# Kernel tuning notes

Hardware: AMD Instinct MI355X
Metric: run time of the kernel (lower is better)

## Reference

```python
import jax, jax.numpy as jnp
import numpy as np

ANG, CEN = 9, 4
MIND, MAXD = -4, 4
NDISP = MAXD - MIND + 1
BDR = CEN * MAXD  # 16
EPS = 1e-5


def lrelu(x):
    return jnp.where(x >= 0, x, 0.1 * x)


def bn(x, p):
    # p: [4, C] = (gamma, beta, running_mean, running_var); inference-mode BatchNorm
    g, b, m, v = p
    sh = (1, -1) + (1,) * (x.ndim - 2)
    return (x - m.reshape(sh)) * (g.reshape(sh) * jax.lax.rsqrt(v.reshape(sh) + EPS)) + b.reshape(sh)


def conv3d(x, w, pad):
    return jax.lax.conv_general_dilated(
        x, w, (1, 1, 1), [(pad[0], pad[0]), (pad[1], pad[1]), (pad[2], pad[2])],
        dimension_numbers=('NCDHW', 'OIDHW', 'NCDHW'))


def pw3d(x, w, b=None):  # 1x1x1 conv
    y = jnp.einsum('oc,bcdhw->bodhw', w, x)
    return y if b is None else y + b.reshape(1, -1, 1, 1, 1)


def bilinear_zeros(img, px, py):
    # torch F.grid_sample(mode='bilinear', padding_mode='zeros', align_corners=False)
    # img [..., h, w]; px, py: same leading dims + [h, w] (pixel coords)
    h, w = img.shape[-2], img.shape[-1]
    x0 = jnp.floor(px); y0 = jnp.floor(py)
    dx = px - x0; dy = py - y0
    x0i = x0.astype(jnp.int32); y0i = y0.astype(jnp.int32)
    flat = img.reshape(img.shape[:-2] + (h * w,))

    def tap(yi, xi, wgt):
        valid = ((xi >= 0) & (xi < w) & (yi >= 0) & (yi < h)).astype(img.dtype)
        idx = jnp.clip(yi, 0, h - 1) * w + jnp.clip(xi, 0, w - 1)
        v = jnp.take_along_axis(flat, idx.reshape(idx.shape[:-2] + (h * w,)), axis=-1)
        return v.reshape(idx.shape) * wgt * valid

    return (tap(y0i, x0i, (1 - dx) * (1 - dy)) + tap(y0i, x0i + 1, dx * (1 - dy)) +
            tap(y0i + 1, x0i, (1 - dx) * dy) + tap(y0i + 1, x0i + 1, dx * dy))


def generate_mask(lf, disp):
    # lf [b,1,9,9,h,w]; warp() is called with -disp in the torch code
    b, _, _, _, h, w = lf.shape
    imgs = lf[:, 0]                                    # [b,9,9,h,w]
    d = -disp[:, 0]                                    # [b,h,w]
    off = (jnp.arange(ANG) - CEN).astype(imgs.dtype)   # du / dv
    xb = jnp.linspace(0.0, 1.0, w).astype(imgs.dtype)
    yb = jnp.linspace(0.0, 1.0, h).astype(imgs.dtype)
    # grid = 2*(base+shift)-1; align_corners=False pixel coord = ((g+1)*S - 1)/2
    px = (xb[None, None, None, :] + off[None, :, None, None] * d[:, None] / w) * w - 0.5  # [b,9(v),h,w]
    py = (yb[None, None, :, None] + off[None, :, None, None] * d[:, None] / h) * h - 0.5  # [b,9(u),h,w]
    PX = jnp.broadcast_to(px[:, None], (b, ANG, ANG, h, w))
    PY = jnp.broadcast_to(py[:, :, None], (b, ANG, ANG, h, w))
    warped = bilinear_zeros(imgs, PX, PY)
    ref = imgs[:, CEN, CEN][:, None, None]
    diff = jnp.abs(warped - ref)
    diff = diff.at[:, CEN, CEN].set(0.0)  # center view is used unwarped -> zero diff
    return ((1.0 - diff) ** 2).reshape(b, ANG * ANG, h, w)


def build_cost(feat, mask, fuse_w):
    # Direct windowed gather equivalent of the per-disparity Unfold(dilation=h_pad-d)
    # on the angular-tiled padded image. For disparity d and view (ki,kj), output
    # pixel (i,j) reads view (ki,kj) at (i+(CEN-ki)*d, j+(CEN-kj)*d), zeros outside.
    b, c, _, h, w = feat.shape                        # feat [b,8,81,h,w]
    f = feat.reshape(b, c, ANG, ANG, h, w)
    fpad = jnp.pad(f, ((0, 0), (0, 0), (0, 0), (0, 0), (BDR, BDR), (BDR, BDR)))
    ds = jnp.arange(MIND, MAXD + 1)                   # [9]
    ki = jnp.arange(ANG)
    row = BDR + (CEN - ki)[None, :, None] * ds[:, None, None] + jnp.arange(h)[None, None, :]  # [D,9,h]
    col = BDR + (CEN - ki)[None, :, None] * ds[:, None, None] + jnp.arange(w)[None, None, :]  # [D,9,w]
    KI = ki[None, :, None, None, None]
    KJ = ki[None, None, :, None, None]
    RR = row[:, :, None, :, None]
    CC = col[:, None, :, None, :]
    g = fpad[:, :, KI, KJ, RR, CC]                    # [b,8,D,9,9,h,w]
    mod = g * mask.reshape(b, 1, 1, ANG, ANG, h, w)   # mask modulation (ModulateConv2d)
    Wf = fuse_w.reshape(c, fuse_w.shape[0] // c, ANG, ANG)  # grouped 1x1 fuse, groups=c
    cost = jnp.einsum('gouv,bgduvhw->bgodhw', Wf, mod).reshape(b, fuse_w.shape[0], NDISP, h, w)
    return cost / mask.mean(axis=1)[:, None, None]


def _forward(x, dispGT, if_w0, if_bn0, resb_w, resb_b, resb_bn, if_w1, if_bn1,
             if_w2, if_bn2, last_w, fuse_w, sq_w, sq_bn, c1_w, c1_bn, c2_w, c2_bn,
             c3_w, c3_bn, c4_w, r3_body_w, r3_body_bn, r3_ca_w1, r3_ca_b1, r3_ca_bn1,
             r3_ca_w2, r3_ca_b2, r3_ca_bn2):
    b = x.shape[0]
    h = x.shape[2] // ANG; w = x.shape[3] // ANG
    lf = x.reshape(b, 1, ANG, h, ANG, w).transpose(0, 1, 2, 4, 3, 5)  # [b,1,a1,a2,h,w]
    x5 = lf.reshape(b, 1, ANG * ANG, h, w)
    # ---- init_feature: per-view 2D convs expressed as (1,3,3) 3D convs
    hbuf = bn(conv3d(x5, if_w0, (0, 1, 1)), if_bn0)
    for i in range(8):  # 8 ResB blocks (fixed architecture depth)
        t = lrelu(bn(conv3d(hbuf, resb_w[i, 0], (0, 1, 1)) + resb_b[i, 0].reshape(1, -1, 1, 1, 1), resb_bn[i, 0]))
        t = bn(conv3d(t, resb_w[i, 1], (0, 1, 1)) + resb_b[i, 1].reshape(1, -1, 1, 1, 1), resb_bn[i, 1])
        hbuf = hbuf + t
    hbuf = lrelu(bn(conv3d(hbuf, if_w1, (0, 1, 1)), if_bn1))
    hbuf = lrelu(bn(conv3d(hbuf, if_w2, (0, 1, 1)), if_bn2))
    feat = conv3d(hbuf, last_w, (0, 1, 1))            # [b,8,81,h,w]
    # ---- occlusion-aware mask + cost volume
    mask = generate_mask(lf, dispGT)                  # [b,81,h,w]
    cost = build_cost(feat, mask, fuse_w)             # [b,512,9,h,w]
    # ---- 3D CNN aggregation
    buf = lrelu(bn(pw3d(cost, sq_w), sq_bn))
    buf = lrelu(bn(conv3d(buf, c1_w, (1, 1, 1)), c1_bn))
    buf = lrelu(bn(conv3d(buf, c2_w, (1, 1, 1)), c2_bn))
    for i in range(2):  # ResB3D blocks with CALayer
        t = lrelu(bn(conv3d(buf, r3_body_w[i, 0], (1, 1, 1)), r3_body_bn[i, 0]))
        t = bn(conv3d(t, r3_body_w[i, 1], (1, 1, 1)), r3_body_bn[i, 1])
        y = t.mean(axis=(3, 4), keepdims=True)        # AdaptiveAvgPool3d((9,1,1))
        y = lrelu(bn(pw3d(y, r3_ca_w1[i], r3_ca_b1[i]), r3_ca_bn1[i]))
        y = jax.nn.sigmoid(bn(pw3d(y, r3_ca_w2[i], r3_ca_b2[i]), r3_ca_bn2[i]))
        buf = t * y + buf
    buf = lrelu(bn(conv3d(buf, c3_w, (1, 1, 1)), c3_bn))
    score = conv3d(buf, c4_w, (1, 1, 1))[:, 0]        # [b,9,h,w]
    att = jax.nn.softmax(score, axis=1)
    dvals = jnp.arange(MIND, MAXD + 1).astype(att.dtype)
    return jnp.sum(att * dvals[None, :, None, None], axis=1, keepdims=True)  # [b,1,h,w]


def setup_inputs():
    B, H, W = 1, 64, 64
    keys = iter(jax.random.split(jax.random.key(0), 256))

    def nrm(shape, fan_in):
        return jax.random.normal(next(keys), shape, jnp.float32) / np.float32(np.sqrt(fan_in))

    def bnp(c):
        k1, k2, k3, k4 = jax.random.split(next(keys), 4)
        return jnp.stack([jax.random.uniform(k1, (c,), jnp.float32, 0.5, 1.5),
                          0.1 * jax.random.normal(k2, (c,), jnp.float32),
                          0.1 * jax.random.normal(k3, (c,), jnp.float32),
                          jax.random.uniform(k4, (c,), jnp.float32, 0.5, 1.5)])

    d = {}
    d['x'] = jax.random.normal(next(keys), (B, 1, ANG * H, ANG * W), jnp.float32)
    d['dispGT'] = jax.random.uniform(next(keys), (B, 1, H, W), jnp.float32, -4.0, 4.0)
    d['if_w0'] = nrm((16, 1, 1, 3, 3), 9)
    d['if_bn0'] = bnp(16)
    d['resb_w'] = nrm((8, 2, 16, 16, 1, 3, 3), 16 * 9)
    d['resb_b'] = 0.01 * jax.random.normal(next(keys), (8, 2, 16), jnp.float32)
    d['resb_bn'] = jnp.stack([jnp.stack([bnp(16), bnp(16)]) for _ in range(8)])
    d['if_w1'] = nrm((16, 16, 1, 3, 3), 16 * 9)
    d['if_bn1'] = bnp(16)
    d['if_w2'] = nrm((8, 16, 1, 3, 3), 16 * 9)
    d['if_bn2'] = bnp(8)
    d['last_w'] = nrm((8, 8, 1, 3, 3), 8 * 9)
    d['fuse_w'] = nrm((512, 81), 81)
    d['sq_w'] = nrm((160, 512), 512)
    d['sq_bn'] = bnp(160)
    for nmn in ('c1', 'c2', 'c3'):
        d[nmn + '_w'] = nrm((160, 160, 3, 3, 3), 160 * 27)
        d[nmn + '_bn'] = bnp(160)
    d['c4_w'] = nrm((1, 160, 3, 3, 3), 160 * 27)
    d['r3_body_w'] = nrm((2, 2, 160, 160, 3, 3, 3), 160 * 27)
    d['r3_body_bn'] = jnp.stack([jnp.stack([bnp(160), bnp(160)]) for _ in range(2)])
    d['r3_ca_w1'] = nrm((2, 10, 160), 160)
    d['r3_ca_b1'] = 0.01 * jax.random.normal(next(keys), (2, 10), jnp.float32)
    d['r3_ca_bn1'] = jnp.stack([bnp(10) for _ in range(2)])
    d['r3_ca_w2'] = nrm((2, 160, 10), 10)
    d['r3_ca_b2'] = 0.01 * jax.random.normal(next(keys), (2, 160), jnp.float32)
    d['r3_ca_bn2'] = jnp.stack([bnp(160) for _ in range(2)])
    return d


def reference(x, dispGT, if_w0, if_bn0, resb_w, resb_b, resb_bn, if_w1, if_bn1,
              if_w2, if_bn2, last_w, fuse_w, sq_w, sq_bn, c1_w, c1_bn, c2_w, c2_bn,
              c3_w, c3_bn, c4_w, r3_body_w, r3_body_bn, r3_ca_w1, r3_ca_b1, r3_ca_bn1,
              r3_ca_w2, r3_ca_b2, r3_ca_bn2):
    return _forward(x, dispGT, if_w0, if_bn0, resb_w, resb_b, resb_bn, if_w1, if_bn1,
                    if_w2, if_bn2, last_w, fuse_w, sq_w, sq_bn, c1_w, c1_bn, c2_w, c2_bn,
                    c3_w, c3_bn, c4_w, r3_body_w, r3_body_bn, r3_ca_w1, r3_ca_b1, r3_ca_bn1,
                    r3_ca_w2, r3_ca_b2, r3_ca_bn2)
```

## Files before the change

### kernel.cpp

```cpp
#include <hip/hip_runtime.h>
#include <hip/hip_bf16.h>
#include <math.h>

constexpr float EPSB = 1e-5f;

constexpr int SAS = 69696;
constexpr int SRS = 1056;
constexpr size_t SVOL = 81ull * SAS;

constexpr int PZS = 696960;
constexpr int PYS = 10560;
constexpr size_t PVOL = 11ull * 4356 * 160;

constexpr size_t OFF_SA   = 0;
constexpr size_t OFF_SB   = 5645376;
constexpr size_t OFF_MASK = 11290752;
constexpr size_t OFF_INVM = 11622528;
constexpr size_t OFF_SC   = 11626624;
constexpr size_t OFF_YM   = 11663488;
constexpr size_t OFF_Y2   = 11664928;
constexpr size_t OFF_YMP  = 11666368;
constexpr size_t OFF_PA   = 11712448;
constexpr size_t UOFF_PHA = 38758016;
constexpr size_t UOFF_PHB = 46424576;
constexpr size_t UOFF_WH  = 54091136;
constexpr size_t UOFF_WSH = 63767936;
constexpr size_t UOFF_ABH = 63865216;
constexpr size_t UOFF_ABL = 63972736;

typedef short s16x8 __attribute__((ext_vector_type(8)));
typedef short s16x4 __attribute__((ext_vector_type(4)));
typedef float f32x4 __attribute__((ext_vector_type(4)));
typedef _Float16 h16x8 __attribute__((ext_vector_type(8)));
typedef _Float16 h16x4 __attribute__((ext_vector_type(4)));

__device__ __forceinline__ float lrelu_f(float v) { return v >= 0.f ? v : 0.1f * v; }
__device__ __forceinline__ float b2f(unsigned short s) {
  union { float f; unsigned u; } z; z.u = ((unsigned)s) << 16; return z.f;
}
__device__ __forceinline__ unsigned short f2b(float f) {
  __hip_bfloat16 h = __float2bfloat16(f);
  return *(unsigned short*)&h;
}

__global__ __launch_bounds__(256) void k_if0(const float* __restrict__ x,
                                             const float* __restrict__ w0,
                                             const float* __restrict__ bn0,
                                             float* __restrict__ SA) {
  int a = blockIdx.x;
  int p = blockIdx.y * 256 + threadIdx.x;
  int y = p >> 6, xx = p & 63;
  int ai = a / 9, aj = a % 9;
  float v[3][3];
#pragma unroll
  for (int dy = 0; dy < 3; ++dy) {
    int gy = y + dy - 1;
#pragma unroll
    for (int dx = 0; dx < 3; ++dx) {
      int gx = xx + dx - 1;
      v[dy][dx] = (gy >= 0 && gy < 64 && gx >= 0 && gx < 64)
                      ? x[(ai * 64 + gy) * 576 + aj * 64 + gx] : 0.f;
    }
  }
  float o16[16];
#pragma unroll
  for (int c = 0; c < 16; ++c) {
    float acc = 0.f;
#pragma unroll
    for (int t = 0; t < 9; ++t) acc += w0[c * 9 + t] * v[t / 3][t % 3];
    float g = bn0[c], b = bn0[16 + c], m = bn0[32 + c], vv = bn0[48 + c];
    o16[c] = (acc - m) * (g * rsqrtf(vv + EPSB)) + b;
  }
  float* dst = SA + (size_t)a * SAS + (size_t)(y + 1) * SRS + (size_t)(xx + 1) * 16;
#pragma unroll
  for (int q = 0; q < 4; ++q)
    *(float4*)&dst[q * 4] = make_float4(o16[q*4], o16[q*4+1], o16[q*4+2], o16[q*4+3]);
}

__global__ __launch_bounds__(256) void k_wslice(const float* __restrict__ resb_w,
                                                const float* __restrict__ if1_w,
                                                const float* __restrict__ if2_w,
                                                const float* __restrict__ last_w,
                                                _Float16* __restrict__ WSH) {
  int c = blockIdx.x;
  for (int idx = threadIdx.x; idx < 2560; idx += 256) {
    int o = idx / 160, k = idx % 160;
    int t = k >> 4, ci = k & 15;
    float v = 0.f;
    if (t < 9) {
      if (c < 16)       v = resb_w[((size_t)c * 256 + o * 16 + ci) * 9 + t];
      else if (c == 16) v = if1_w[(size_t)(o * 16 + ci) * 9 + t];
      else if (c == 17) v = (o < 8) ? if2_w[(size_t)(o * 16 + ci) * 9 + t] : 0.f;
      else              v = (o < 8 && ci < 8) ? last_w[(size_t)(o * 8 + ci) * 9 + t] : 0.f;
    }
    WSH[c * 2560 + idx] = (_Float16)v;
  }
}

__global__ __launch_bounds__(256) void k_wt7(const float* __restrict__ c1,
                                             const float* __restrict__ c2,
                                             const float* __restrict__ r3,
                                             const float* __restrict__ c3,
                                             _Float16* __restrict__ WH) {
  __shared__ float L[6912];
  int l = blockIdx.y;
  const float* w = (l == 0) ? c1 : (l == 1) ? c2 : (l < 6) ? r3 + (size_t)(l - 2) * 691200 : c3;
  size_t base = (size_t)blockIdx.x * 256;
  for (int i = threadIdx.x; i < 6912; i += 256) L[i] = w[base * 27 + i];
  __syncthreads();
  _Float16* wh = WH + (size_t)l * 691200;
  int r = (int)base + threadIdx.x;
#pragma unroll 1
  for (int t = 0; t < 27; ++t) {
    float v = L[threadIdx.x * 27 + t];
    wh[(size_t)t * 25600 + r] = (_Float16)v;
  }
}

__global__ __launch_bounds__(192) void k_A(const float* __restrict__ sq_w,
                                           const float* __restrict__ fuse_w,
                                           unsigned short* __restrict__ ABH,
                                           unsigned short* __restrict__ ABL) {
  int k = blockIdx.x;
  int o = threadIdx.x;
  if (o >= 160) return;
  float acc = 0.f;
  if (k < 648) {
    int uv = k >> 3, g = k & 7;
    for (int o2 = 0; o2 < 64; ++o2)
      acc += sq_w[(size_t)o * 512 + g * 64 + o2] * fuse_w[(size_t)(g * 64 + o2) * 81 + uv];
  }
  unsigned short h = f2b(acc);
  ABH[(size_t)o * 672 + k] = h;
  ABL[(size_t)o * 672 + k] = f2b(acc - b2f(h));
}

__device__ __forceinline__ float img_at(const float* __restrict__ x, int i, int j, int yy, int xx) {
  if (yy < 0 || yy >= 64 || xx < 0 || xx >= 64) return 0.f;
  return x[(i * 64 + yy) * 576 + j * 64 + xx];
}

__global__ __launch_bounds__(256) void k_mask(const float* __restrict__ x,
                                              const float* __restrict__ disp,
                                              float* __restrict__ mask,
                                              float* __restrict__ invm) {
  int p = blockIdx.x * 256 + threadIdx.x;
  int y = p >> 6, xx = p & 63;
  float d = -disp[p];
  float ref = x[(4 * 64 + y) * 576 + 4 * 64 + xx];
  float ssum = 0.f;
  float xbase = (float)xx * (64.0f / 63.0f);
  float ybase = (float)y * (64.0f / 63.0f);
  for (int i = 0; i < 9; ++i) {
    float py = ybase + (float)(i - 4) * d - 0.5f;
    float y0f = floorf(py);
    float fy = py - y0f;
    int y0 = (int)y0f;
    for (int j = 0; j < 9; ++j) {
      float px = xbase + (float)(j - 4) * d - 0.5f;
      float x0f = floorf(px);
      float fx = px - x0f;
      int x0 = (int)x0f;
      float val = img_at(x, i, j, y0, x0) * (1.f - fx) * (1.f - fy)
                + img_at(x, i, j, y0, x0 + 1) * fx * (1.f - fy)
                + img_at(x, i, j, y0 + 1, x0) * (1.f - fx) * fy
                + img_at(x, i, j, y0 + 1, x0 + 1) * fx * fy;
      float diff = (i == 4 && j == 4) ? 0.f : fabsf(val - ref);
      float m = 1.f - diff;
      m = m * m;
      mask[(i * 9 + j) * 4096 + p] = m;
      ssum += m;
    }
  }
  invm[p] = 81.f / ssum;
}

template <bool BN, bool LRELU, bool RESADD, int CO>
__global__ __launch_bounds__(256) void k_cs(const float* __restrict__ in,
                                            float* __restrict__ out,
                                            const _Float16* __restrict__ wsh,
                                            const float* __restrict__ bias,
                                            const float* __restrict__ bnp) {
  __shared__ _Float16 Af[15840];
  int a = blockIdx.x, y0 = blockIdx.y * 8;
  int tid = threadIdx.x, lane = tid & 63, w = tid >> 6;
  int lr = lane & 15, lq = lane >> 4;
  const float* src = in + (size_t)a * SAS + (size_t)y0 * SRS;
  for (int it = tid; it < 2640; it += 256) {
    int row = it / 264, rem = it % 264;
    float4 f = *(const float4*)&src[row * SRS + rem * 4];
    int px = rem >> 2, q = rem & 3;
    h16x4 hv;
    hv[0] = (_Float16)f.x;
    hv[1] = (_Float16)f.y;
    hv[2] = (_Float16)f.z;
    hv[3] = (_Float16)f.w;
    *(h16x4*)&Af[(row * 66 + px) * 24 + q * 4] = hv;
  }
  __syncthreads();
  h16x8 bh[5];
#pragma unroll
  for (int ks = 0; ks < 5; ++ks)
    bh[ks] = *(const h16x8*)&wsh[lr * 160 + ks * 32 + lq * 8];
  int offk[5];
#pragma unroll
  for (int ks = 0; ks < 5; ++ks) {
    int t = ks * 2 + (lq >> 1);
    if (t > 8) t = 8;
    offk[ks] = ((t / 3) * 66 + (t % 3)) * 24 + (lq & 1) * 8;
  }
  f32x4 acc[8];
#pragma unroll
  for (int i = 0; i < 8; ++i) acc[i] = (f32x4){0.f, 0.f, 0.f, 0.f};
#pragma unroll
  for (int mf = 0; mf < 8; ++mf) {
    int gm = w * 8 + mf;
    int yl = gm >> 2, xq = gm & 3;
    int am = (yl * 66 + xq * 16 + lr) * 24;
#pragma unroll
    for (int ks = 0; ks < 5; ++ks) {
      h16x8 ah = *(const h16x8*)&Af[am + offk[ks]];
      acc[mf] = __builtin_amdgcn_mfma_f32_16x16x32_f16(ah, bh[ks], acc[mf], 0, 0, 0);
    }
  }
  int co = lr;
  bool coval = (CO == 16) || (co < CO);
  float sc = 1.f, sh = 0.f;
  if (BN && coval) {
    float g = bnp[co], b = bnp[CO + co], m = bnp[2 * CO + co], vv = bnp[3 * CO + co];
    sc = g * rsqrtf(vv + EPSB);
    sh = b - m * sc;
    if (bias) sh += bias[co] * sc;
  }
#pragma unroll
  for (int mf = 0; mf < 8; ++mf) {
    int gm = w * 8 + mf;
    int yl = gm >> 2, xq = gm & 3;
    if (coval) {
#pragma unroll
      for (int r = 0; r < 4; ++r) {
        int x = xq * 16 + lq * 4 + r;
        float val = acc[mf][r] * sc + sh;
        if (LRELU) val = lrelu_f(val);
        size_t oo = (size_t)a * SAS + (size_t)(y0 + yl + 1) * SRS + (size_t)(x + 1) * 16 + co;
        if (RESADD) out[oo] += val;
        else        out[oo] = val;
      }
    }
  }
}

__global__ __launch_bounds__(256) void k_costsq(const float* __restrict__ feat,
                                                const float* __restrict__ mask,
                                                const float* __restrict__ invm,
                                                const unsigned short* __restrict__ ABH,
                                                const unsigned short* __restrict__ ABL,
                                                const float* __restrict__ sq_bn,
                                                _Float16* __restrict__ outPH) {
  __shared__ short Ah[6144];
  __shared__ short Al[6144];
  int dI = blockIdx.x, y = blockIdx.y;
  int dd = dI - 4;
  int tid = threadIdx.x, lane = tid & 63, w = tid >> 6;
  int wm = w >> 1, wn = w & 1;
  int lr = lane & 15, lq = lane >> 4;
  f32x4 acc[2][5];
#pragma unroll
  for (int i = 0; i < 2; ++i)
#pragma unroll
    for (int j = 0; j < 5; ++j) acc[i][j] = (f32x4){0.f, 0.f, 0.f, 0.f};

  for (int ch = 0; ch < 7; ++ch) {
    __syncthreads();
    for (int it = tid; it < 768; it += 256) {
      int xl = it / 12, uvL = it % 12;
      int uv = ch * 12 + uvL;
      s16x8 hv = {0, 0, 0, 0, 0, 0, 0, 0}, lv = {0, 0, 0, 0, 0, 0, 0, 0};
      if (uv < 81) {
        int u = uv / 9, v = uv % 9;
        int ys = y + (4 - u) * dd;
        int xs = xl + (4 - v) * dd;
        if (ys >= 0 && ys < 64 && xs >= 0 && xs < 64) {
          const float* fp = feat + (size_t)uv * SAS + (size_t)(ys + 1) * SRS + (size_t)(xs + 1) * 16;
          float mv = mask[uv * 4096 + y * 64 + xl];
#pragma unroll
          for (int j = 0; j < 8; ++j) {
            float f = fp[j] * mv;
            unsigned short h = f2b(f);
            hv[j] = h;
            lv[j] = f2b(f - b2f(h));
          }
        }
      }
      *(s16x8*)&Ah[xl * 96 + uvL * 8] = hv;
      *(s16x8*)&Al[xl * 96 + uvL * 8] = lv;
    }
    __syncthreads();
#pragma unroll
    for (int kb = 0; kb < 3; ++kb) {
      int ka = kb * 32 + lq * 8;
      s16x8 a0h = *(const s16x8*)&Ah[(wm * 32 + lr) * 96 + ka];
      s16x8 a0l = *(const s16x8*)&Al[(wm * 32 + lr) * 96 + ka];
      s16x8 a1h = *(const s16x8*)&Ah[(wm * 32 + 16 + lr) * 96 + ka];
      s16x8 a1l = *(const s16x8*)&Al[(wm * 32 + 16 + lr) * 96 + ka];
      int kg = ch * 96 + ka;
#pragma unroll
      for (int nf = 0; nf < 5; ++nf) {
        int n = wn * 80 + nf * 16 + lr;
        s16x8 bh = *(const s16x8*)&ABH[(size_t)n * 672 + kg];
        s16x8 bl = *(const s16x8*)&ABL[(size_t)n * 672 + kg];
        acc[0][nf] = __builtin_amdgcn_mfma_f32_16x16x32_bf16(a0h, bh, acc[0][nf], 0, 0, 0);
        acc[0][nf] = __builtin_amdgcn_mfma_f32_16x16x32_bf16(a0h, bl, acc[0][nf], 0, 0, 0);
        acc[0][nf] = __builtin_amdgcn_mfma_f32_16x16x32_bf16(a0l, bh, acc[0][nf], 0, 0, 0);
        acc[1][nf] = __builtin_amdgcn_mfma_f32_16x16x32_bf16(a1h, bh, acc[1][nf], 0, 0, 0);
        acc[1][nf] = __builtin_amdgcn_mfma_f32_16x16x32_bf16(a1h, bl, acc[1][nf], 0, 0, 0);
        acc[1][nf] = __builtin_amdgcn_mfma_f32_16x16x32_bf16(a1l, bh, acc[1][nf], 0, 0, 0);
      }
    }
  }
#pragma unroll
  for (int nf = 0; nf < 5; ++nf) {
    int n = wn * 80 + nf * 16 + lr;
    float g = sq_bn[n], b = sq_bn[160 + n], m = sq_bn[320 + n], vv = sq_bn[480 + n];
    float sc = g * rsqrtf(vv + EPSB), sh = b - m * sc;
#pragma unroll
    for (int mf = 0; mf < 2; ++mf) {
#pragma unroll
      for (int r = 0; r < 4; ++r) {
        int x = wm * 32 + mf * 16 + lq * 4 + r;
        float val = acc[mf][nf][r] * invm[y * 64 + x];
        val = val * sc + sh;
        val = lrelu_f(val);
        outPH[(size_t)(dI + 1) * PZS + (size_t)(y + 1) * PYS + (size_t)(x + 1) * 160 + n] =
            (_Float16)val;
      }
    }
  }
}

template <bool LRELU>
__global__ __launch_bounds__(320, 3) void k_mconv(const _Float16* __restrict__ in,
                                                  float* __restrict__ out32,
                                                  _Float16* __restrict__ out16,
                                                  const _Float16* __restrict__ wh,
                                                  const float* __restrict__ bnp) {
  __shared__ _Float16 Af[66 * 168];
  int bid = blockIdx.x;
  int swz = (bid & 7) * 72 + (bid >> 3);
  int z = swz / 64, y = swz % 64;
  int tid = threadIdx.x;
  int lane = tid & 63;
  int wn = tid >> 6;
  int lr = lane & 15;
  int lq = lane >> 4;

  f32x4 acc[4][2];
#pragma unroll
  for (int i = 0; i < 4; ++i)
#pragma unroll
    for (int j = 0; j < 2; ++j) acc[i][j] = (f32x4){0.f, 0.f, 0.f, 0.f};

  const _Float16* wbase = wh + (size_t)(wn * 32 + lr) * 160 + lq * 8;

#pragma unroll 1
  for (int dzy = 0; dzy < 9; ++dzy) {
    int dz = dzy / 3, dy = dzy % 3;
    const _Float16* src = in + (size_t)(z + dz) * PZS + (size_t)(y + dy) * PYS;
    __syncthreads();
    for (int v = tid; v < 1320; v += 320) {
      h16x8 g = *(const h16x8*)&src[(size_t)v * 8];
      int row = v / 20, col = (v % 20) * 8;
      *(h16x8*)&Af[row * 168 + col] = g;
    }
    __syncthreads();

#pragma unroll 1
    for (int dx = 0; dx < 3; ++dx) {
      const _Float16* wt = wbase + (size_t)(dzy * 3 + dx) * 25600;
      h16x8 bA[2], bB[2];
#pragma unroll
      for (int nf = 0; nf < 2; ++nf)
        bA[nf] = *(const h16x8*)&wt[(size_t)nf * 16 * 160];

      auto step = [&](int ks, h16x8 (&cur)[2], h16x8 (&nxt)[2], bool pre) {
        if (pre) {
#pragma unroll
          for (int nf = 0; nf < 2; ++nf)
            nxt[nf] = *(const h16x8*)&wt[(size_t)nf * 16 * 160 + (ks + 1) * 32];
        }
        h16x8 a0 = *(const h16x8*)&Af[(0 * 16 + lr + dx) * 168 + ks * 32 + lq * 8];
        h16x8 a1 = *(const h16x8*)&Af[(1 * 16 + lr + dx) * 168 + ks * 32 + lq * 8];
        h16x8 a2 = *(const h16x8*)&Af[(2 * 16 + lr + dx) * 168 + ks * 32 + lq * 8];
        h16x8 a3 = *(const h16x8*)&Af[(3 * 16 + lr + dx) * 168 + ks * 32 + lq * 8];
#pragma unroll
        for (int nf = 0; nf < 2; ++nf) {
          acc[0][nf] = __builtin_amdgcn_mfma_f32_16x16x32_f16(a0, cur[nf], acc[0][nf], 0, 0, 0);
          acc[1][nf] = __builtin_amdgcn_mfma_f32_16x16x32_f16(a1, cur[nf], acc[1][nf], 0, 0, 0);
          acc[2][nf] = __builtin_amdgcn_mfma_f32_16x16x32_f16(a2, cur[nf], acc[2][nf], 0, 0, 0);
          acc[3][nf] = __builtin_amdgcn_mfma_f32_16x16x32_f16(a3, cur[nf], acc[3][nf], 0, 0, 0);
        }
      };
      step(0, bA, bB, true);
      step(1, bB, bA, true);
      step(2, bA, bB, true);
      step(3, bB, bA, true);
      step(4, bA, bB, false);
    }
  }
#pragma unroll
  for (int nf = 0; nf < 2; ++nf) {
    int n = wn * 32 + nf * 16 + lr;
    float sc = bnp[n] * rsqrtf(bnp[480 + n] + EPSB);
    float sh = bnp[160 + n] - bnp[320 + n] * sc;
#pragma unroll
    for (int mq = 0; mq < 4; ++mq) {
#pragma unroll
      for (int r = 0; r < 4; ++r) {
        int x = mq * 16 + lq * 4 + r;
        float val = acc[mq][nf][r] * sc + sh;
        if (LRELU) val = lrelu_f(val);
        size_t oo = (size_t)(z + 1) * PZS + (size_t)(y + 1) * PYS + (size_t)(x + 1) * 160 + n;
        if (out32) out32[oo] = val;
        if (out16) out16[oo] = (_Float16)val;
      }
    }
  }
}

__global__ __launch_bounds__(256) void k_c4(const _Float16* __restrict__ in,
                                            const float* __restrict__ w,
                                            float* __restrict__ score) {
  __shared__ float L[66 * 169];
  __shared__ float red[256];
  int zy = blockIdx.x;
  int z = zy / 64, y = zy % 64;
  int tid = threadIdx.x;
  int x = tid & 63, q = tid >> 6;
  float acc = 0.f;
  for (int dzy = 0; dzy < 9; ++dzy) {
    int dz = dzy / 3, dy = dzy % 3;
    const _Float16* src = in + (size_t)(z + dz) * PZS + (size_t)(y + dy) * PYS;
    __syncthreads();
    for (int v = tid; v < 1320; v += 256) {
      h16x8 g = *(const h16x8*)&src[v * 8];
      int row = v / 20, col = (v % 20) * 8;
#pragma unroll
      for (int j = 0; j < 8; ++j) L[row * 169 + col + j] = (float)g[j];
    }
    __syncthreads();
#pragma unroll 1
    for (int dx = 0; dx < 3; ++dx) {
      int t = dzy * 3 + dx;
      for (int ci = q * 40; ci < q * 40 + 40; ++ci)
        acc += L[(x + dx) * 169 + ci] * w[ci * 27 + t];
    }
  }
  red[tid] = acc;
  __syncthreads();
  if (q == 0)
    score[z * 4096 + y * 64 + x] = red[x] + red[64 + x] + red[128 + x] + red[192 + x];
}

__global__ __launch_bounds__(256) void k_mean1(const float* __restrict__ in,
                                               float* __restrict__ ymp) {
  int z = blockIdx.x, yg = blockIdx.y, xq = blockIdx.z;
  int c = threadIdx.x;
  if (c >= 160) return;
  float s = 0.f;
  for (int yy = 0; yy < 8; ++yy) {
    int y = yg * 8 + yy;
    for (int xl = 0; xl < 16; ++xl) {
      int x = xq * 16 + xl;
      s += in[(size_t)(z + 1) * PZS + (size_t)(y + 1) * PYS + (size_t)(x + 1) * 160 + c];
    }
  }
  ymp[((z * 8 + yg) * 4 + xq) * 160 + c] = s;
}

__global__ __launch_bounds__(256) void k_mean2(const float* __restrict__ ymp,
                                               float* __restrict__ ym) {
  int idx = blockIdx.x * 256 + threadIdx.x;
  if (idx >= 1440) return;
  int c = idx / 9, z = idx % 9;
  float s = 0.f;
  for (int p = 0; p < 32; ++p) s += ymp[(z * 32 + p) * 160 + c];
  ym[idx] = s * (1.f / 4096.f);
}

__global__ __launch_bounds__(256) void k_ca(const float* __restrict__ ym,
                                            const float* __restrict__ w1,
                                            const float* __restrict__ b1,
                                            const float* __restrict__ bn1,
                                            const float* __restrict__ w2,
                                            const float* __restrict__ b2,
                                            const float* __restrict__ bn2,
                                            float* __restrict__ y2) {
  __shared__ float yml[1440];
  __shared__ float yy[90];
  for (int i = threadIdx.x; i < 1440; i += 256) yml[i] = ym[i];
  __syncthreads();
  if (threadIdx.x < 90) {
    int c = threadIdx.x / 9, z = threadIdx.x % 9;
    float acc = b1[c];
    for (int ci = 0; ci < 160; ++ci) acc += w1[c * 160 + ci] * yml[ci * 9 + z];
    float g = bn1[c], b = bn1[10 + c], m = bn1[20 + c], vv = bn1[30 + c];
    acc = (acc - m) * (g * rsqrtf(vv + EPSB)) + b;
    yy[threadIdx.x] = lrelu_f(acc);
  }
  __syncthreads();
  for (int i = threadIdx.x; i < 1440; i += 256) {
    int c = i / 9, z = i % 9;
    float acc = b2[c];
#pragma unroll
    for (int k = 0; k < 10; ++k) acc += w2[c * 10 + k] * yy[k * 9 + z];
    float g = bn2[c], b = bn2[160 + c], m = bn2[320 + c], vv = bn2[480 + c];
    acc = (acc - m) * (g * rsqrtf(vv + EPSB)) + b;
    y2[i] = 1.f / (1.f + expf(-acc));
  }
}

__global__ __launch_bounds__(256) void k_sadd(float* __restrict__ buf,
                                              _Float16* __restrict__ shadow,
                                              const float* __restrict__ t,
                                              const float* __restrict__ y2) {
  int i = blockIdx.x * 256 + threadIdx.x;
  int p = i / 160, c = i % 160;
  int z = p >> 12, r = p & 4095;
  int y = r >> 6, x = r & 63;
  size_t a = (size_t)(z + 1) * PZS + (size_t)(y + 1) * PYS + (size_t)(x + 1) * 160 + c;
  float val = buf[a] + t[a] * y2[c * 9 + z];
  buf[a] = val;
  shadow[a] = (_Float16)val;
}

__global__ __launch_bounds__(256) void k_out(const float* __restrict__ score,
                                             float* __restrict__ out) {
  int p = blockIdx.x * 256 + threadIdx.x;
  float v[9];
  float mx = -1e30f;
#pragma unroll
  for (int z = 0; z < 9; ++z) {
    v[z] = score[z * 4096 + p];
    mx = fmaxf(mx, v[z]);
  }
  float s = 0.f, r = 0.f;
#pragma unroll
  for (int z = 0; z < 9; ++z) {
    float e = expf(v[z] - mx);
    s += e;
    r += e * (float)(z - 4);
  }
  out[p] = r / s;
}

extern "C" void kernel_launch(void* const* d_in, const int* in_sizes, int n_in,
                              void* d_out, int out_size, void* d_ws, size_t ws_size,
                              hipStream_t stream) {
  const float* X      = (const float*)d_in[0];
  const float* disp   = (const float*)d_in[1];
  const float* if_w0  = (const float*)d_in[2];
  const float* if_bn0 = (const float*)d_in[3];
  const float* resb_w = (const float*)d_in[4];
  const float* resb_b = (const float*)d_in[5];
  const float* resb_bn= (const float*)d_in[6];
  const float* if_w1  = (const float*)d_in[7];
  const float* if_bn1 = (const float*)d_in[8];
  const float* if_w2  = (const float*)d_in[9];
  const float* if_bn2 = (const float*)d_in[10];
  const float* last_w = (const float*)d_in[11];
  const float* fuse_w = (const float*)d_in[12];
  const float* sq_w   = (const float*)d_in[13];
  const float* sq_bn  = (const float*)d_in[14];
  const float* c1_w   = (const float*)d_in[15];
  const float* c1_bn  = (const float*)d_in[16];
  const float* c2_w   = (const float*)d_in[17];
  const float* c2_bn  = (const float*)d_in[18];
  const float* c3_w   = (const float*)d_in[19];
  const float* c3_bn  = (const float*)d_in[20];
  const float* c4_w   = (const float*)d_in[21];
  const float* r3_w   = (const float*)d_in[22];
  const float* r3_bn  = (const float*)d_in[23];
  const float* ca_w1  = (const float*)d_in[24];
  const float* ca_b1  = (const float*)d_in[25];
  const float* ca_bn1 = (const float*)d_in[26];
  const float* ca_w2  = (const float*)d_in[27];
  const float* ca_b2  = (const float*)d_in[28];
  const float* ca_bn2 = (const float*)d_in[29];

  float* ws   = (float*)d_ws;
  float* SA   = ws + OFF_SA;
  float* SB   = ws + OFF_SB;
  float* PC   = ws;
  float* MASK = ws + OFF_MASK;
  float* INVM = ws + OFF_INVM;
  float* SC   = ws + OFF_SC;
  float* YM   = ws + OFF_YM;
  float* Y2   = ws + OFF_Y2;
  float* YMP  = ws + OFF_YMP;
  float* PA   = ws + OFF_PA;
  unsigned short* U   = (unsigned short*)d_ws;
  _Float16* PHA       = (_Float16*)(U + UOFF_PHA);
  _Float16* PHB       = (_Float16*)(U + UOFF_PHB);
  _Float16* WH        = (_Float16*)(U + UOFF_WH);
  _Float16* WSS       = (_Float16*)(U + UOFF_WSH);
  unsigned short* ABH = U + UOFF_ABH;
  unsigned short* ABL = U + UOFF_ABL;

  hipMemsetAsync(SA, 0, SVOL * 4, stream);
  hipMemsetAsync(SB, 0, SVOL * 4, stream);
  hipMemsetAsync(PHA, 0, PVOL * 2, stream);
  hipMemsetAsync(PHB, 0, PVOL * 2, stream);

  k_wt7<<<dim3(100, 7), 256, 0, stream>>>(c1_w, c2_w, r3_w, c3_w, WH);
  k_wslice<<<19, 256, 0, stream>>>(resb_w, if_w1, if_w2, last_w, WSS);
  k_A<<<672, 192, 0, stream>>>(sq_w, fuse_w, ABH, ABL);
  k_mask<<<16, 256, 0, stream>>>(X, disp, MASK, INVM);

  k_if0<<<dim3(81, 16), 256, 0, stream>>>(X, if_w0, if_bn0, SA);
  for (int i = 0; i < 8; ++i) {
    k_cs<true, true, false, 16><<<dim3(81, 8), 256, 0, stream>>>(
        SA, SB, WSS + (size_t)(2 * i) * 2560, resb_b + i * 32, resb_bn + i * 128);
    k_cs<true, false, true, 16><<<dim3(81, 8), 256, 0, stream>>>(
        SB, SA, WSS + (size_t)(2 * i + 1) * 2560, resb_b + i * 32 + 16, resb_bn + i * 128 + 64);
  }
  k_cs<true, true, false, 16><<<dim3(81, 8), 256, 0, stream>>>(
      SA, SB, WSS + 16 * 2560, nullptr, if_bn1);
  k_cs<true, true, false, 8><<<dim3(81, 8), 256, 0, stream>>>(
      SB, SA, WSS + 17 * 2560, nullptr, if_bn2);
  k_cs<false, false, false, 8><<<dim3(81, 8), 256, 0, stream>>>(
      SA, SB, WSS + 18 * 2560, nullptr, nullptr);

  k_costsq<<<dim3(9, 64), 256, 0, stream>>>(SB, MASK, INVM, ABH, ABL, sq_bn, PHA);

  k_mconv<true><<<576, 320, 0, stream>>>(PHA, nullptr, PHB, WH + 0ull * 691200, c1_bn);
  k_mconv<true><<<576, 320, 0, stream>>>(PHB, PA, PHA, WH + 1ull * 691200, c2_bn);
  for (int i = 0; i < 2; ++i) {
    k_mconv<true><<<576, 320, 0, stream>>>(PHA, nullptr, PHB,
                                           WH + (size_t)(2 + 2 * i) * 691200, r3_bn + i * 1280);
    k_mconv<false><<<576, 320, 0, stream>>>(PHB, PC, nullptr,
                                            WH + (size_t)(3 + 2 * i) * 691200,
                                            r3_bn + i * 1280 + 640);
    k_mean1<<<dim3(9, 8, 4), 256, 0, stream>>>(PC, YMP);
    k_mean2<<<6, 256, 0, stream>>>(YMP, YM);
    k_ca<<<1, 256, 0, stream>>>(YM, ca_w1 + i * 1600, ca_b1 + i * 10, ca_bn1 + i * 40,
                                ca_w2 + i * 1600, ca_b2 + i * 160, ca_bn2 + i * 640, Y2);
    k_sadd<<<23040, 256, 0, stream>>>(PA, PHA, PC, Y2);
  }
  k_mconv<true><<<576, 320, 0, stream>>>(PHA, nullptr, PHB, WH + 6ull * 691200, c3_bn);
  k_c4<<<576, 256, 0, stream>>>(PHB, c4_w, SC);
  k_out<<<16, 256, 0, stream>>>(SC, (float*)d_out);
}
```

Before: 1.019 ms.

## Store feature-extractor activations in fp16 and pad LDS rows against bank conflicts

The 2D feature-extraction stage (k_if0, k_cs chain, k_costsq input) now keeps its padded activation buffers in fp16 instead of fp32. This halves global traffic and memset size for those buffers and removes the per-load conversion in k_cs. LDS row strides in k_cs and k_mconv are also widened (24→26, 168→174) to reduce shared-memory bank conflicts. The cost is precision: residual accumulation across 8 blocks now rounds to fp16 after every add.

New measurement: 980.8 us. 3.8% less time.

```diff
diff --git a/kernel.cpp b/kernel.cpp
--- a/kernel.cpp
+++ b/kernel.cpp
@@ -23,13 +23,14 @@
 constexpr size_t OFF_PA   = 11712448;
 constexpr size_t UOFF_PHA = 38758016;
 constexpr size_t UOFF_PHB = 46424576;
+constexpr size_t UOFF_SHA = 0;
+constexpr size_t UOFF_SHB = 11290752;
 constexpr size_t UOFF_WH  = 54091136;
 constexpr size_t UOFF_WSH = 63767936;
 constexpr size_t UOFF_ABH = 63865216;
 constexpr size_t UOFF_ABL = 63972736;
 
 typedef short s16x8 __attribute__((ext_vector_type(8)));
-typedef short s16x4 __attribute__((ext_vector_type(4)));
 typedef float f32x4 __attribute__((ext_vector_type(4)));
 typedef _Float16 h16x8 __attribute__((ext_vector_type(8)));
 typedef _Float16 h16x4 __attribute__((ext_vector_type(4)));
@@ -46,7 +47,7 @@
 __global__ __launch_bounds__(256) void k_if0(const float* __restrict__ x,
                                              const float* __restrict__ w0,
                                              const float* __restrict__ bn0,
-                                             float* __restrict__ SA) {
+                                             _Float16* __restrict__ SHA) {
   int a = blockIdx.x;
   int p = blockIdx.y * 256 + threadIdx.x;
   int y = p >> 6, xx = p & 63;
@@ -62,19 +63,20 @@
                       ? x[(ai * 64 + gy) * 576 + aj * 64 + gx] : 0.f;
     }
   }
-  float o16[16];
+  h16x8 o0, o1;
 #pragma unroll
   for (int c = 0; c < 16; ++c) {
     float acc = 0.f;
 #pragma unroll
     for (int t = 0; t < 9; ++t) acc += w0[c * 9 + t] * v[t / 3][t % 3];
     float g = bn0[c], b = bn0[16 + c], m = bn0[32 + c], vv = bn0[48 + c];
-    o16[c] = (acc - m) * (g * rsqrtf(vv + EPSB)) + b;
-  }
-  float* dst = SA + (size_t)a * SAS + (size_t)(y + 1) * SRS + (size_t)(xx + 1) * 16;
-#pragma unroll
-  for (int q = 0; q < 4; ++q)
-    *(float4*)&dst[q * 4] = make_float4(o16[q*4], o16[q*4+1], o16[q*4+2], o16[q*4+3]);
+    float val = (acc - m) * (g * rsqrtf(vv + EPSB)) + b;
+    if (c < 8) o0[c] = (_Float16)val;
+    else       o1[c - 8] = (_Float16)val;
+  }
+  _Float16* dst = SHA + (size_t)a * SAS + (size_t)(y + 1) * SRS + (size_t)(xx + 1) * 16;
+  *(h16x8*)&dst[0] = o0;
+  *(h16x8*)&dst[8] = o1;
 }
 
 __global__ __launch_bounds__(256) void k_wslice(const float* __restrict__ resb_w,
@@ -176,26 +178,21 @@
 }
 
 template <bool BN, bool LRELU, bool RESADD, int CO>
-__global__ __launch_bounds__(256) void k_cs(const float* __restrict__ in,
-                                            float* __restrict__ out,
+__global__ __launch_bounds__(256) void k_cs(const _Float16* __restrict__ in,
+                                            _Float16* __restrict__ out,
                                             const _Float16* __restrict__ wsh,
                                             const float* __restrict__ bias,
                                             const float* __restrict__ bnp) {
-  __shared__ _Float16 Af[15840];
+  __shared__ _Float16 Af[10 * 66 * 26];
   int a = blockIdx.x, y0 = blockIdx.y * 8;
   int tid = threadIdx.x, lane = tid & 63, w = tid >> 6;
   int lr = lane & 15, lq = lane >> 4;
-  const float* src = in + (size_t)a * SAS + (size_t)y0 * SRS;
-  for (int it = tid; it < 2640; it += 256) {
-    int row = it / 264, rem = it % 264;
-    float4 f = *(const float4*)&src[row * SRS + rem * 4];
-    int px = rem >> 2, q = rem & 3;
-    h16x4 hv;
-    hv[0] = (_Float16)f.x;
-    hv[1] = (_Float16)f.y;
-    hv[2] = (_Float16)f.z;
-    hv[3] = (_Float16)f.w;
-    *(h16x4*)&Af[(row * 66 + px) * 24 + q * 4] = hv;
+  const _Float16* src = in + (size_t)a * SAS + (size_t)y0 * SRS;
+  for (int it = tid; it < 1320; it += 256) {
+    int row = it / 132, rem = it % 132;
+    int px = rem >> 1, half = rem & 1;
+    h16x8 g = *(const h16x8*)&src[row * SRS + px * 16 + half * 8];
+    *(h16x8*)&Af[(row * 66 + px) * 26 + half * 8] = g;
   }
   __syncthreads();
   h16x8 bh[5];
@@ -207,7 +204,7 @@
   for (int ks = 0; ks < 5; ++ks) {
     int t = ks * 2 + (lq >> 1);
     if (t > 8) t = 8;
-    offk[ks] = ((t / 3) * 66 + (t % 3)) * 24 + (lq & 1) * 8;
+    offk[ks] = ((t / 3) * 66 + (t % 3)) * 26 + (lq & 1) * 8;
   }
   f32x4 acc[8];
 #pragma unroll
@@ -216,7 +213,7 @@
   for (int mf = 0; mf < 8; ++mf) {
     int gm = w * 8 + mf;
     int yl = gm >> 2, xq = gm & 3;
-    int am = (yl * 66 + xq * 16 + lr) * 24;
+    int am = (yl * 66 + xq * 16 + lr) * 26;
 #pragma unroll
     for (int ks = 0; ks < 5; ++ks) {
       h16x8 ah = *(const h16x8*)&Af[am + offk[ks]];
@@ -243,14 +240,14 @@
         float val = acc[mf][r] * sc + sh;
         if (LRELU) val = lrelu_f(val);
         size_t oo = (size_t)a * SAS + (size_t)(y0 + yl + 1) * SRS + (size_t)(x + 1) * 16 + co;
-        if (RESADD) out[oo] += val;
-        else        out[oo] = val;
+        if (RESADD) out[oo] = (_Float16)((float)out[oo] + val);
+        else        out[oo] = (_Float16)val;
       }
     }
   }
 }
 
-__global__ __launch_bounds__(256) void k_costsq(const float* __restrict__ feat,
+__global__ __launch_bounds__(256) void k_costsq(const _Float16* __restrict__ feat,
                                                 const float* __restrict__ mask,
                                                 const float* __restrict__ invm,
                                                 const unsigned short* __restrict__ ABH,
@@ -281,11 +278,12 @@
         int ys = y + (4 - u) * dd;
         int xs = xl + (4 - v) * dd;
         if (ys >= 0 && ys < 64 && xs >= 0 && xs < 64) {
-          const float* fp = feat + (size_t)uv * SAS + (size_t)(ys + 1) * SRS + (size_t)(xs + 1) * 16;
+          const _Float16* fp = feat + (size_t)uv * SAS + (size_t)(ys + 1) * SRS + (size_t)(xs + 1) * 16;
+          h16x8 fv = *(const h16x8*)fp;
           float mv = mask[uv * 4096 + y * 64 + xl];
 #pragma unroll
           for (int j = 0; j < 8; ++j) {
-            float f = fp[j] * mv;
+            float f = (float)fv[j] * mv;
             unsigned short h = f2b(f);
             hv[j] = h;
             lv[j] = f2b(f - b2f(h));
@@ -344,7 +342,7 @@
                                                   _Float16* __restrict__ out16,
                                                   const _Float16* __restrict__ wh,
                                                   const float* __restrict__ bnp) {
-  __shared__ _Float16 Af[66 * 168];
+  __shared__ _Float16 Af[66 * 174];
   int bid = blockIdx.x;
   int swz = (bid & 7) * 72 + (bid >> 3);
   int z = swz / 64, y = swz % 64;
@@ -370,7 +368,7 @@
     for (int v = tid; v < 1320; v += 320) {
       h16x8 g = *(const h16x8*)&src[(size_t)v * 8];
       int row = v / 20, col = (v % 20) * 8;
-      *(h16x8*)&Af[row * 168 + col] = g;
+      *(h16x8*)&Af[row * 174 + col] = g;
     }
     __syncthreads();
 
@@ -388,10 +386,10 @@
           for (int nf = 0; nf < 2; ++nf)
             nxt[nf] = *(const h16x8*)&wt[(size_t)nf * 16 * 160 + (ks + 1) * 32];
         }
-        h16x8 a0 = *(const h16x8*)&Af[(0 * 16 + lr + dx) * 168 + ks * 32 + lq * 8];
-        h16x8 a1 = *(const h16x8*)&Af[(1 * 16 + lr + dx) * 168 + ks * 32 + lq * 8];
-        h16x8 a2 = *(const h16x8*)&Af[(2 * 16 + lr + dx) * 168 + ks * 32 + lq * 8];
-        h16x8 a3 = *(const h16x8*)&Af[(3 * 16 + lr + dx) * 168 + ks * 32 + lq * 8];
+        h16x8 a0 = *(const h16x8*)&Af[(0 * 16 + lr + dx) * 174 + ks * 32 + lq * 8];
+        h16x8 a1 = *(const h16x8*)&Af[(1 * 16 + lr + dx) * 174 + ks * 32 + lq * 8];
+        h16x8 a2 = *(const h16x8*)&Af[(2 * 16 + lr + dx) * 174 + ks * 32 + lq * 8];
+        h16x8 a3 = *(const h16x8*)&Af[(3 * 16 + lr + dx) * 174 + ks * 32 + lq * 8];
 #pragma unroll
         for (int nf = 0; nf < 2; ++nf) {
           acc[0][nf] = __builtin_amdgcn_mfma_f32_16x16x32_f16(a0, cur[nf], acc[0][nf], 0, 0, 0);
@@ -588,8 +586,6 @@
   const float* ca_bn2 = (const float*)d_in[29];
 
   float* ws   = (float*)d_ws;
-  float* SA   = ws + OFF_SA;
-  float* SB   = ws + OFF_SB;
   float* PC   = ws;
   float* MASK = ws + OFF_MASK;
   float* INVM = ws + OFF_INVM;
@@ -599,6 +595,8 @@
   float* YMP  = ws + OFF_YMP;
   float* PA   = ws + OFF_PA;
   unsigned short* U   = (unsigned short*)d_ws;
+  _Float16* SHA       = (_Float16*)(U + UOFF_SHA);
+  _Float16* SHB       = (_Float16*)(U + UOFF_SHB);
   _Float16* PHA       = (_Float16*)(U + UOFF_PHA);
   _Float16* PHB       = (_Float16*)(U + UOFF_PHB);
   _Float16* WH        = (_Float16*)(U + UOFF_WH);
@@ -606,8 +604,8 @@
   unsigned short* ABH = U + UOFF_ABH;
   unsigned short* ABL = U + UOFF_ABL;
 
-  hipMemsetAsync(SA, 0, SVOL * 4, stream);
-  hipMemsetAsync(SB, 0, SVOL * 4, stream);
+  hipMemsetAsync(SHA, 0, SVOL * 2, stream);
+  hipMemsetAsync(SHB, 0, SVOL * 2, stream);
   hipMemsetAsync(PHA, 0, PVOL * 2, stream);
   hipMemsetAsync(PHB, 0, PVOL * 2, stream);
 
@@ -616,21 +614,21 @@
   k_A<<<672, 192, 0, stream>>>(sq_w, fuse_w, ABH, ABL);
   k_mask<<<16, 256, 0, stream>>>(X, disp, MASK, INVM);
 
-  k_if0<<<dim3(81, 16), 256, 0, stream>>>(X, if_w0, if_bn0, SA);
+  k_if0<<<dim3(81, 16), 256, 0, stream>>>(X, if_w0, if_bn0, SHA);
   for (int i = 0; i < 8; ++i) {
     k_cs<true, true, false, 16><<<dim3(81, 8), 256, 0, stream>>>(
-        SA, SB, WSS + (size_t)(2 * i) * 2560, resb_b + i * 32, resb_bn + i * 128);
+        SHA, SHB, WSS + (size_t)(2 * i) * 2560, resb_b + i * 32, resb_bn + i * 128);
     k_cs<true, false, true, 16><<<dim3(81, 8), 256, 0, stream>>>(
-        SB, SA, WSS + (size_t)(2 * i + 1) * 2560, resb_b + i * 32 + 16, resb_bn + i * 128 + 64);
+        SHB, SHA, WSS + (size_t)(2 * i + 1) * 2560, resb_b + i * 32 + 16, resb_bn + i * 128 + 64);
   }
   k_cs<true, true, false, 16><<<dim3(81, 8), 256, 0, stream>>>(
-      SA, SB, WSS + 16 * 2560, nullptr, if_bn1);
+      SHA, SHB, WSS + 16 * 2560, nullptr, if_bn1);
   k_cs<true, true, false, 8><<<dim3(81, 8), 256, 0, stream>>>(
-      SB, SA, WSS + 17 * 2560, nullptr, if_bn2);
+      SHB, SHA, WSS + 17 * 2560, nullptr, if_bn2);
   k_cs<false, false, false, 8><<<dim3(81, 8), 256, 0, stream>>>(
-      SA, SB, WSS + 18 * 2560, nullptr, nullptr);
-
-  k_costsq<<<dim3(9, 64), 256, 0, stream>>>(SB, MASK, INVM, ABH, ABL, sq_bn, PHA);
+      SHA, SHB, WSS + 18 * 2560, nullptr, nullptr);
+
+  k_costsq<<<dim3(9, 64), 256, 0, stream>>>(SHB, MASK, INVM, ABH, ABL, sq_bn, PHA);
 
   k_mconv<true><<<576, 320, 0, stream>>>(PHA, nullptr, PHB, WH + 0ull * 691200, c1_bn);
   k_mconv<true><<<576, 320, 0, stream>>>(PHB, PA, PHA, WH + 1ull * 691200, c2_bn);
```
